# Kernel tuning notes

Hardware: AMD Instinct MI355X
Metric: run time of the kernel (lower is better)

The kernel has to match this reference:

```python
import jax, jax.numpy as jnp
import numpy as np

EPS = 1e-7
CURVS = (1.0, 0.8, 1.2)
SCALES = (1.0, 0.8, 0.6)


def expmap0(v, c):
    sc = jnp.sqrt(c)
    n = jnp.maximum(jnp.linalg.norm(v, axis=-1, keepdims=True), EPS)
    return jnp.tanh(sc * n) * v / (sc * n)


def projx(x, c):
    max_n = (1.0 - 1e-5) / jnp.sqrt(c)
    n = jnp.maximum(jnp.linalg.norm(x, axis=-1, keepdims=True), EPS)
    return jnp.where(n > max_n, x * (max_n / n), x)


def logmap0(x, c):
    sc = jnp.sqrt(c)
    n = jnp.maximum(jnp.linalg.norm(x, axis=-1, keepdims=True), EPS)
    a = jnp.clip(sc * n, 0.0, 1.0 - 1e-7)
    return jnp.arctanh(a) * x / (sc * n)


def hamilton(q1, q2):
    # q1, q2: [..., 4] (w,x,y,z), broadcasting allowed
    w1, x1, y1, z1 = q1[..., 0], q1[..., 1], q1[..., 2], q1[..., 3]
    w2, x2, y2, z2 = q2[..., 0], q2[..., 1], q2[..., 2], q2[..., 3]
    w = w1 * w2 - x1 * x2 - y1 * y2 - z1 * z2
    x = w1 * x2 + x1 * w2 + y1 * z2 - z1 * y2
    y = w1 * y2 - x1 * z2 + y1 * w2 + z1 * x2
    z = w1 * z2 + x1 * y2 - y1 * x2 + z1 * w2
    return jnp.stack([w, x, y, z], axis=-1)


def mlp(v, Wa, ba, Wb, bb):
    # Linear -> GELU(exact, matching torch default) -> Linear; dropout is eval-mode identity
    return jax.nn.gelu(v @ Wa.T + ba, approximate=False) @ Wb.T + bb


def setup_inputs() -> dict:
    key = jax.random.key(0)
    ks = jax.random.split(key, 24)
    f32 = jnp.float32
    B = 65536
    d = {}
    d['x'] = jax.random.normal(ks[0], (B, 784), dtype=f32)
    # input embedding 784 -> 128, then to level-0 tangent space 128 -> 64
    d['W_in'] = jax.random.normal(ks[1], (128, 784), f32) * (1.0 / np.sqrt(784))
    d['b_in'] = jnp.zeros((128,), f32)
    d['W_tan'] = jax.random.normal(ks[2], (64, 128), f32) * (1.0 / np.sqrt(128))
    d['b_tan'] = jnp.zeros((64,), f32)
    # boundary-manifold tangent points per level (init_scale=0.01 as in BoundaryManifold)
    d['bp0'] = jax.random.normal(ks[3], (5, 64), f32) * 0.01
    d['bp1'] = jax.random.normal(ks[4], (3, 4), f32) * 0.01
    d['bp2'] = jax.random.normal(ks[5], (4, 32), f32) * 0.01
    # rotation 0->1: SO(64) via matrix exponential of a skew-symmetric generator
    d['A_rot'] = jax.random.normal(ks[6], (64, 64), f32) * 0.02
    # rotation 1->2: SO(4) via pvq unit quaternions (std=0.1 init as in source)
    d['p_quat'] = jax.random.normal(ks[7], (4,), f32) * 0.1
    d['q_quat'] = jax.random.normal(ks[8], (4,), f32) * 0.1
    # inter-level MLP transform 0->1: 64 -> 32 -> 4
    d['W0a'] = jax.random.normal(ks[9], (32, 64), f32) * (1.0 / np.sqrt(64))
    d['b0a'] = jnp.zeros((32,), f32)
    d['W0b'] = jax.random.normal(ks[10], (4, 32), f32) * (1.0 / np.sqrt(32))
    d['b0b'] = jnp.zeros((4,), f32)
    # inter-level MLP transform 1->2: 4 -> 16 -> 32
    d['W1a'] = jax.random.normal(ks[11], (16, 4), f32) * (1.0 / np.sqrt(4))
    d['b1a'] = jnp.zeros((16,), f32)
    d['W1b'] = jax.random.normal(ks[12], (32, 16), f32) * (1.0 / np.sqrt(16))
    d['b1b'] = jnp.zeros((32,), f32)
    # output head: concat_tangent (64+4+32=100) -> 10
    d['W_out'] = jax.random.normal(ks[13], (10, 100), f32) * (1.0 / np.sqrt(100))
    d['b_out'] = jnp.zeros((10,), f32)
    return d


def reference(x, W_in, b_in, W_tan, b_tan, bp0, bp1, bp2, A_rot, p_quat, q_quat,
              W0a, b0a, W0b, b0b, W1a, b1a, W1b, b1b, W_out, b_out):
    h = x @ W_in.T + b_in                       # [B, 128]
    v = h @ W_tan.T + b_tan                     # [B, 64] level-0 tangent vector
    bps = (bp0, bp1, bp2)
    level_tangents = []
    carried = None                              # boundary tangent vectors transformed from prev level
    for i in range(3):
        c, s = CURVS[i], SCALES[i]
        # scaled exp/log round trip through the Poincare ball of this level
        x_hyp = projx(expmap0(v * s, c), c)
        v_tan = logmap0(x_hyp, c) / s           # [B, d_i]
        # boundary manifold: tangent -> ball -> proj -> tangent
        b_own = logmap0(projx(expmap0(bps[i], c), c), c)  # [P_i, d_i]
        bnds = b_own if carried is None else jnp.concatenate([b_own, carried], axis=0)
        # relative vectors vs boundary points, mean-aggregated
        rel_agg = v_tan.mean(axis=0, keepdims=False) * 0 + (v_tan[:, None, :] - bnds[None, :, :]).mean(axis=1)  # [B, d_i]
        level_tangents.append(v_tan)
        v_comb = v_tan + rel_agg
        if i == 0:
            R = jax.scipy.linalg.expm(A_rot - A_rot.T)   # SO(64)
            v_rot = v_comb @ R.T
            b_rot = bnds @ R.T
            v = mlp(v_rot, W0a, b0a, W0b, b0b)
            carried = mlp(b_rot, W0a, b0a, W0b, b0b)
        elif i == 1:
            p = p_quat / (jnp.linalg.norm(p_quat) + EPS)
            q = q_quat / (jnp.linalg.norm(q_quat) + EPS)
            v_rot = hamilton(hamilton(p, v_comb), q)     # pvq SO(4) rotation
            b_rot = hamilton(hamilton(p, bnds), q)
            v = mlp(v_rot, W1a, b1a, W1b, b1b)
            carried = mlp(b_rot, W1a, b1a, W1b, b1b)
    agg = jnp.concatenate(level_tangents, axis=-1)       # [B, 100] concat_tangent
    return agg @ W_out.T + b_out                         # [B, 10]
```

## Files before the change

kernel.cpp:

```cpp
#include <hip/hip_runtime.h>
#include <hip/hip_bf16.h>

typedef __attribute__((ext_vector_type(4))) float f32x4;
typedef __attribute__((ext_vector_type(2))) unsigned int u32x2;
typedef __attribute__((ext_vector_type(4))) unsigned int u32x4;
typedef __attribute__((ext_vector_type(8))) short bf16x8;

#define EPSF 1e-7f

__device__ __forceinline__ float radial_factor(float sumsq, float c, float s){
  float sc = sqrtf(c);
  float nv = sqrtf(sumsq);
  float nu = fmaxf(s*nv, EPSF);
  float th = tanhf(sc*nu);
  float r1 = th/sc;
  float maxn = (1.0f - 1e-5f)/sc;
  float r2 = fminf(r1, maxn);
  float n1 = fmaxf(r2, EPSF);
  float a  = fminf(sc*n1, 1.0f - 1e-7f);
  float r3 = 0.5f*logf((1.0f + a)/(1.0f - a));
  return r3*r2/(sc*n1*nu);
}

__device__ __forceinline__ float gelu_f(float x){
  return 0.5f*x*(1.0f + erff(x*0.70710678118654752f));
}

__device__ __forceinline__ unsigned f2bf1(float f){
  unsigned u = __float_as_uint(f);
  return (u + 0x7FFFu + ((u>>16)&1u)) >> 16;
}
__device__ __forceinline__ unsigned f2bf_pk(float lo, float hi){
  unsigned ul = f2bf1(lo);
  unsigned uh = __float_as_uint(hi);
  uh = (uh + 0x7FFFu + ((uh>>16)&1u)) & 0xFFFF0000u;
  return ul | uh;
}

#define WS_WC     0
#define WS_BCOMB  204800
#define WS_W0AE   205056
#define WS_BROT0  213248
#define WS_BOWN0  214528
#define WS_W0AT   215808
#define WS_MB0    224000
#define WS_MB1    224256
#define WS_W1AE   224272

__global__ __launch_bounds__(256) void prep_a(
    const float* __restrict__ W_in, const float* __restrict__ b_in,
    const float* __restrict__ W_tan, const float* __restrict__ b_tan,
    const float* __restrict__ A_rot, const float* __restrict__ W0a,
    const float* __restrict__ bp0,
    unsigned short* __restrict__ Wc, float* __restrict__ bcomb,
    float* __restrict__ W0aE, float* __restrict__ brot0, float* __restrict__ bown0)
{
  __shared__ __align__(16) float Al[64][68];
  __shared__ __align__(16) float ST[64][68];
  const int bid = blockIdx.x, t = threadIdx.x;

  if (bid < 50){
    if (bid == 0 && t < 64){
      float s = b_tan[t];
      for (int j = 0; j < 128; ++j) s += b_in[j]*W_tan[t*128+j];
      bcomb[t] = s;
    }
    const int g4 = bid*256 + t;
    const int n = g4/200, k4 = (g4 - n*200)*4;
    f32x4 s = {0.f,0.f,0.f,0.f};
    if (k4 < 784){
      for (int j = 0; j < 128; ++j){
        float wt = W_tan[n*128+j];
        f32x4 wi = *(const f32x4*)(W_in + j*784 + k4);
        s += wt*wi;
      }
    }
    u32x2 st = { f2bf_pk(s[0], s[1]), f2bf_pk(s[2], s[3]) };
    *(u32x2*)(Wc + n*800 + k4) = st;
  } else {
    for (int m = t; m < 4096; m += 256){
      int r = m >> 6, c = m & 63;
      Al[r][c] = A_rot[m];
    }
    __syncthreads();
    for (int m = t; m < 4096; m += 256){
      int r = m >> 6, c = m & 63;
      ST[r][c] = Al[c][r] - Al[r][c];
    }
    __syncthreads();
    const int wv = t >> 6, lane = t & 63;
    const int row = (bid - 50)*4 + wv;
    if (row < 37){
      float v, sgn;
      if (row < 32){ v = W0a[row*64 + lane]; sgn = 1.f; }
      else {
        const int r = row - 32;
        float b = bp0[r*64 + lane];
        float ssq = b*b;
        #pragma unroll
        for (int d = 1; d < 64; d <<= 1) ssq += __shfl_xor(ssq, d);
        float fc = radial_factor(ssq, 1.0f, 1.0f);
        v = b*fc;
        bown0[r*64 + lane] = v;
        sgn = -1.f;
      }
      float acc = v;
      for (int k = 1; k <= 12; ++k){
        const float coef = sgn/(float)k;
        float nv = 0.f;
        #pragma unroll
        for (int m = 0; m < 64; m += 4){
          f32x4 s4 = *(const f32x4*)&ST[lane][m];
          nv += __int_as_float(__builtin_amdgcn_readlane(__float_as_int(v), m+0))*s4[0];
          nv += __int_as_float(__builtin_amdgcn_readlane(__float_as_int(v), m+1))*s4[1];
          nv += __int_as_float(__builtin_amdgcn_readlane(__float_as_int(v), m+2))*s4[2];
          nv += __int_as_float(__builtin_amdgcn_readlane(__float_as_int(v), m+3))*s4[3];
        }
        nv *= coef;
        v = nv; acc += nv;
      }
      if (row < 32) W0aE[row*64 + lane] = acc;
      else          brot0[(row-32)*64 + lane] = acc;
    }
  }
}

__global__ __launch_bounds__(256) void prep_small(
    const float* __restrict__ bp1,
    const float* __restrict__ p_quat, const float* __restrict__ q_quat,
    const float* __restrict__ b0a, const float* __restrict__ W0b, const float* __restrict__ b0b,
    const float* __restrict__ W1a,
    const float* __restrict__ W0aE, const float* __restrict__ brot0, const float* __restrict__ bown0,
    float* __restrict__ W0aT, float* __restrict__ mb0, float* __restrict__ mb1,
    float* __restrict__ W1aE)
{
  __shared__ float g[5][32];
  __shared__ float c1[5][4];
  __shared__ float fac1[3];
  __shared__ float Mq[4][4];
  const int t = threadIdx.x;

  for (int i = t; i < 2048; i += 256){
    int o = i >> 6, k = i & 63;
    W0aT[k*32 + o] = W0aE[i];
  }
  if (t < 64){
    float s = 0.f;
    for (int r = 0; r < 5; ++r) s += bown0[r*64 + t];
    mb0[t] = s * 0.2f;
  }
  if (t < 160){
    int r = t >> 5, o = t & 31;
    float s = b0a[o];
    for (int k = 0; k < 64; ++k) s += brot0[r*64+k]*W0aE[o*64+k];
    g[r][o] = gelu_f(s);
  }
  if (t >= 192 && t < 195){
    int r = t - 192;
    float ssq = 0.f;
    for (int j = 0; j < 4; ++j){ float b = bp1[r*4+j]; ssq += b*b; }
    fac1[r] = radial_factor(ssq, 0.8f, 1.0f);
  }
  if (t == 224){
    float pw=p_quat[0],px=p_quat[1],py=p_quat[2],pz=p_quat[3];
    float n1 = sqrtf(pw*pw+px*px+py*py+pz*pz) + EPSF;
    pw/=n1; px/=n1; py/=n1; pz/=n1;
    float qw=q_quat[0],qx=q_quat[1],qy=q_quat[2],qz=q_quat[3];
    float n2 = sqrtf(qw*qw+qx*qx+qy*qy+qz*qz) + EPSF;
    qw/=n2; qx/=n2; qy/=n2; qz/=n2;
    float Lp[4][4] = {{pw,-px,-py,-pz},{px,pw,-pz,py},{py,pz,pw,-px},{pz,-py,px,pw}};
    float Rq[4][4] = {{qw,-qx,-qy,-qz},{qx,qw,qz,-qy},{qy,-qz,qw,qx},{qz,qy,-qx,qw}};
    #pragma unroll
    for (int i = 0; i < 4; ++i)
      #pragma unroll
      for (int k = 0; k < 4; ++k){
        float s = 0.f;
        #pragma unroll
        for (int m = 0; m < 4; ++m) s += Rq[i][m]*Lp[m][k];
        Mq[i][k] = s;
      }
  }
  __syncthreads();
  if (t < 20){
    int r = t >> 2, o = t & 3;
    float s = b0b[o];
    for (int k = 0; k < 32; ++k) s += g[r][k]*W0b[o*32+k];
    c1[r][o] = s;
  }
  __syncthreads();
  if (t < 4){
    float s = 0.f;
    for (int r = 0; r < 3; ++r) s += bp1[r*4+t]*fac1[r];
    for (int r = 0; r < 5; ++r) s += c1[r][t];
    mb1[t] = s * 0.125f;
  }
  if (t >= 64 && t < 128){
    int i = t - 64, o = i >> 2, kq = i & 3;
    float s = 0.f;
    #pragma unroll
    for (int j = 0; j < 4; ++j) s += W1a[o*4+j]*Mq[j][kq];
    W1aE[o*4+kq] = s;
  }
}

__global__ __launch_bounds__(256, 3) void main_fused(
    const float* __restrict__ x,
    const unsigned short* __restrict__ Wc,
    const float* __restrict__ bcomb,
    const float* __restrict__ W0aT,
    const float* __restrict__ mb0g, const float* __restrict__ mb1g,
    const float* __restrict__ W1aEg,
    const float* __restrict__ b0a, const float* __restrict__ W0b, const float* __restrict__ b0b,
    const float* __restrict__ b1a, const float* __restrict__ W1b, const float* __restrict__ b1b,
    const float* __restrict__ Wout, const float* __restrict__ bout,
    float* __restrict__ out)
{
  __shared__ __align__(16) char smem[49472];
  float* vlds   = (float*)smem;
  float* cWoutS = (float*)(smem + 19456);
  float* cmb0S  = (float*)(smem + 23456);
  float* cW0bS  = (float*)(smem + 23712);
  float* cW1aES = (float*)(smem + 24224);
  float* cb0aS  = (float*)(smem + 24480);
  float* cb0bS  = (float*)(smem + 24608);
  float* cmb1S  = (float*)(smem + 24624);
  float* cb1aS  = (float*)(smem + 24640);
  float* cb1bS  = (float*)(smem + 24704);
  float* cboutS = (float*)(smem + 24832);
  unsigned short* xs  = (unsigned short*)(smem + 24896);
  unsigned short* wsb = (unsigned short*)(smem + 24896 + 10240);
  float* gv     = (float*)(smem + 24896);
  float* g1     = (float*)(smem + 34112);
  float* cW0aTS = (float*)(smem + 39232);
  float* cW1bS  = (float*)(smem + 47424);

  const int tid = threadIdx.x;
  const size_t rowBase = (size_t)blockIdx.x * 64;

  if (tid < 64)  cmb0S[tid] = mb0g[tid];
  if (tid < 32)  cb0aS[tid] = b0a[tid];
  if (tid < 128) cW0bS[tid] = W0b[tid];
  if (tid < 4)   { cb0bS[tid] = b0b[tid]; cmb1S[tid] = mb1g[tid]; }
  if (tid < 64)  cW1aES[tid] = W1aEg[tid];
  if (tid < 16)  cb1aS[tid] = b1a[tid];
  if (tid < 32)  cb1bS[tid] = b1b[tid];
  if (tid < 10)  cboutS[tid] = bout[tid];
  for (int i = tid; i < 1000; i += 256) cWoutS[i] = Wout[i];

  const int lane = tid & 63;
  const int w    = tid >> 6;
  const int wr   = w >> 1, wc = w & 1;
  const int lr   = lane & 15, lkg = lane >> 4;

  const char* gpd[3]; int lod[3]; int advd[3]; int thrd[3]; int isxd[3];
  #pragma unroll
  for (int d = 0; d < 3; ++d){
    const int c = w*3 + d;
    if (c < 8){
      const int row = c*8 + (lane >> 3), seg = lane & 7;
      gpd[d]  = (const char*)(x + (rowBase + (size_t)row)*784 + seg*4);
      lod[d]  = row*40 + seg*4;
      advd[d] = 128;
      thrd[d] = 784 - seg*4;
      isxd[d] = 1;
    } else {
      const int row = (c - 8)*16 + (lane >> 2), seg = lane & 3;
      gpd[d]  = (const char*)(Wc + (size_t)row*800 + seg*8);
      lod[d]  = row*40 + seg*8;
      advd[d] = 64;
      thrd[d] = 1 << 30;
      isxd[d] = 0;
    }
  }
  const int aof0 = (wr*32 + lr)*40 + lkg*8;
  const int aof1 = aof0 + 16*40;
  const int bof0 = (wc*32 + lr)*40 + lkg*8;
  const int bof1 = bof0 + 16*40;

  #pragma unroll
  for (int d = 0; d < 3; ++d){
    u32x4 v = *(const u32x4*)gpd[d];
    gpd[d] += advd[d];
    if (isxd[d]){
      f32x4 f = __builtin_bit_cast(f32x4, v);
      u32x2 p = { f2bf_pk(f[0], f[1]), f2bf_pk(f[2], f[3]) };
      *(u32x2*)(xs + lod[d]) = p;
    } else {
      *(u32x4*)(wsb + lod[d]) = v;
    }
  }
  __syncthreads();

  f32x4 acc00 = {}, acc01 = {}, acc10 = {}, acc11 = {};
  for (int t = 0; t < 25; ++t){
    const int cur = t & 1;
    const bool have = (t < 24);
    u32x4 sv0 = {0,0,0,0}, sv1 = {0,0,0,0}, sv2 = {0,0,0,0};
    if (have){
      const int k0n = (t + 1)*32;
      if (k0n < thrd[0]) sv0 = *(const u32x4*)gpd[0];
      if (k0n < thrd[1]) sv1 = *(const u32x4*)gpd[1];
      if (k0n < thrd[2]) sv2 = *(const u32x4*)gpd[2];
      gpd[0] += advd[0]; gpd[1] += advd[1]; gpd[2] += advd[2];
    }
    const unsigned short* xc = xs  + cur*2560;
    const unsigned short* wcb = wsb + cur*2560;
    bf16x8 a0 = *(const bf16x8*)(xc  + aof0);
    bf16x8 a1 = *(const bf16x8*)(xc  + aof1);
    bf16x8 b0 = *(const bf16x8*)(wcb + bof0);
    bf16x8 b1 = *(const bf16x8*)(wcb + bof1);
    acc00 = __builtin_amdgcn_mfma_f32_16x16x32_bf16(a0, b0, acc00, 0, 0, 0);
    acc01 = __builtin_amdgcn_mfma_f32_16x16x32_bf16(a0, b1, acc01, 0, 0, 0);
    acc10 = __builtin_amdgcn_mfma_f32_16x16x32_bf16(a1, b0, acc10, 0, 0, 0);
    acc11 = __builtin_amdgcn_mfma_f32_16x16x32_bf16(a1, b1, acc11, 0, 0, 0);
    if (have){
      unsigned short* xn = xs  + (cur ^ 1)*2560;
      unsigned short* wn = wsb + (cur ^ 1)*2560;
      if (isxd[0]){ f32x4 f = __builtin_bit_cast(f32x4, sv0);
        u32x2 p = { f2bf_pk(f[0], f[1]), f2bf_pk(f[2], f[3]) }; *(u32x2*)(xn + lod[0]) = p; }
      else { *(u32x4*)(wn + lod[0]) = sv0; }
      if (isxd[1]){ f32x4 f = __builtin_bit_cast(f32x4, sv1);
        u32x2 p = { f2bf_pk(f[0], f[1]), f2bf_pk(f[2], f[3]) }; *(u32x2*)(xn + lod[1]) = p; }
      else { *(u32x4*)(wn + lod[1]) = sv1; }
      if (isxd[2]){ f32x4 f = __builtin_bit_cast(f32x4, sv2);
        u32x2 p = { f2bf_pk(f[0], f[1]), f2bf_pk(f[2], f[3]) }; *(u32x2*)(xn + lod[2]) = p; }
      else { *(u32x4*)(wn + lod[2]) = sv2; }
    }
    __syncthreads();
  }

  {
    f32x4 accA[2][2] = { {acc00, acc01}, {acc10, acc11} };
    #pragma unroll
    for (int fi = 0; fi < 2; ++fi){
      #pragma unroll
      for (int fj = 0; fj < 2; ++fj){
        const int col = wc*32 + fj*16 + lr;
        const int r0  = wr*32 + fi*16 + lkg*4;
        const float bc = bcomb[col];
        #pragma unroll
        for (int j = 0; j < 4; ++j)
          vlds[(r0 + j)*76 + col] = accA[fi][fj][j] + bc;
      }
    }
  }
  for (int i = tid; i < 2048; i += 256) cW0aTS[i] = W0aT[i];
  for (int i = tid; i < 512;  i += 256) cW1bS[i]  = W1b[i];
  __syncthreads();

  const int row = tid >> 2, p4 = tid & 3;

  {
    f32x4 rv[4];
    float* vptr = &vlds[row*76 + p4*16];
    #pragma unroll
    for (int i = 0; i < 4; ++i) rv[i] = ((const f32x4*)vptr)[i];
    float ssq = 0.f;
    #pragma unroll
    for (int i = 0; i < 4; ++i)
      ssq += rv[i][0]*rv[i][0] + rv[i][1]*rv[i][1] + rv[i][2]*rv[i][2] + rv[i][3]*rv[i][3];
    ssq += __shfl_xor(ssq, 1); ssq += __shfl_xor(ssq, 2);
    const float fac = radial_factor(ssq, 1.0f, 1.0f);
    #pragma unroll
    for (int i = 0; i < 4; ++i){ rv[i] *= fac; ((f32x4*)vptr)[i] = rv[i]; }
  }
  __syncthreads();

  {
    const int og = p4;
    float a0o[8];
    #pragma unroll
    for (int j = 0; j < 8; ++j) a0o[j] = cb0aS[og*8 + j];
    #pragma unroll 4
    for (int k = 0; k < 64; k += 4){
      f32x4 vtv = *(const f32x4*)&vlds[row*76 + k];
      f32x4 mm  = *(const f32x4*)&cmb0S[k];
      #pragma unroll
      for (int u = 0; u < 4; ++u){
        const float vc = 2.f*vtv[u] - mm[u];
        const f32x4* wp = (const f32x4*)&cW0aTS[(k+u)*32 + og*8];
        f32x4 w0 = wp[0], w1 = wp[1];
        #pragma unroll
        for (int j = 0; j < 4; ++j){ a0o[j] += w0[j]*vc; a0o[4+j] += w1[j]*vc; }
      }
    }
    #pragma unroll
    for (int j = 0; j < 8; ++j) gv[row*36 + og*8 + j] = gelu_f(a0o[j]);
  }
  __syncthreads();

  {
    const int o1 = p4;
    float a1 = cb0bS[o1];
    #pragma unroll
    for (int k = 0; k < 32; k += 4){
      f32x4 gg = *(const f32x4*)&gv[row*36 + k];
      f32x4 ww = *(const f32x4*)&cW0bS[o1*32 + k];
      a1 += gg[0]*ww[0] + gg[1]*ww[1] + gg[2]*ww[2] + gg[3]*ww[3];
    }
    float ss1 = a1*a1;
    ss1 += __shfl_xor(ss1, 1); ss1 += __shfl_xor(ss1, 2);
    const float f1v = radial_factor(ss1, 0.8f, 0.8f);
    const float vt1 = a1*f1v;
    vlds[row*76 + 64 + o1] = vt1;
    vlds[row*76 + 68 + o1] = 2.f*vt1 - cmb1S[o1];
  }
  __syncthreads();

  {
    const f32x4 vc1 = *(const f32x4*)&vlds[row*76 + 68];
    #pragma unroll
    for (int j = 0; j < 4; ++j){
      const int o = p4*4 + j;
      float s1 = cb1aS[o] + cW1aES[o*4+0]*vc1[0] + cW1aES[o*4+1]*vc1[1]
                          + cW1aES[o*4+2]*vc1[2] + cW1aES[o*4+3]*vc1[3];
      g1[row*20 + o] = gelu_f(s1);
    }
  }
  __syncthreads();

  {
    float v2[8]; float ss2 = 0.f;
    #pragma unroll
    for (int j = 0; j < 8; ++j){
      const int o = p4*8 + j;
      float s = cb1bS[o];
      #pragma unroll
      for (int k = 0; k < 16; k += 4){
        f32x4 gg = *(const f32x4*)&g1[row*20 + k];
        f32x4 ww = *(const f32x4*)&cW1bS[o*16 + k];
        s += gg[0]*ww[0] + gg[1]*ww[1] + gg[2]*ww[2] + gg[3]*ww[3];
      }
      v2[j] = s; ss2 += s*s;
    }
    ss2 += __shfl_xor(ss2, 1); ss2 += __shfl_xor(ss2, 2);
    const float f2v = radial_factor(ss2, 1.2f, 0.6f);
    #pragma unroll
    for (int j = 0; j < 8; ++j) gv[row*36 + p4*8 + j] = v2[j]*f2v;
  }
  __syncthreads();

  for (int idx = tid; idx < 640; idx += 256){
    const int r6 = idx/10, o = idx - r6*10;
    float s = cboutS[o];
    const float* wrow = &cWoutS[o*100];
    const float* vrow = &vlds[r6*76];
    #pragma unroll 4
    for (int k = 0; k < 68; k += 4){
      f32x4 a = *(const f32x4*)(vrow + k);
      f32x4 b = *(const f32x4*)(wrow + k);
      s += a[0]*b[0] + a[1]*b[1] + a[2]*b[2] + a[3]*b[3];
    }
    const float* v2row = &gv[r6*36];
    #pragma unroll 4
    for (int k = 0; k < 32; k += 4){
      f32x4 a = *(const f32x4*)(v2row + k);
      f32x4 b = *(const f32x4*)(wrow + 68 + k);
      s += a[0]*b[0] + a[1]*b[1] + a[2]*b[2] + a[3]*b[3];
    }
    out[(rowBase + (size_t)r6)*10 + o] = s;
  }
}

extern "C" void kernel_launch(void* const* d_in, const int* in_sizes, int n_in,
                              void* d_out, int out_size, void* d_ws, size_t ws_size,
                              hipStream_t stream)
{
  (void)n_in; (void)out_size; (void)ws_size;
  const float* x      = (const float*)d_in[0];
  const float* W_in   = (const float*)d_in[1];
  const float* b_in   = (const float*)d_in[2];
  const float* W_tan  = (const float*)d_in[3];
  const float* b_tan  = (const float*)d_in[4];
  const float* bp0    = (const float*)d_in[5];
  const float* bp1    = (const float*)d_in[6];
  const float* A_rot  = (const float*)d_in[8];
  const float* p_quat = (const float*)d_in[9];
  const float* q_quat = (const float*)d_in[10];
  const float* W0a    = (const float*)d_in[11];
  const float* b0a    = (const float*)d_in[12];
  const float* W0b    = (const float*)d_in[13];
  const float* b0b    = (const float*)d_in[14];
  const float* W1a    = (const float*)d_in[15];
  const float* b1a    = (const float*)d_in[16];
  const float* W1b    = (const float*)d_in[17];
  const float* b1b    = (const float*)d_in[18];
  const float* W_out  = (const float*)d_in[19];
  const float* b_out  = (const float*)d_in[20];

  char* ws = (char*)d_ws;
  unsigned short* Wc = (unsigned short*)(ws + WS_WC);
  float* bcomb = (float*)(ws + WS_BCOMB);
  float* W0aE  = (float*)(ws + WS_W0AE);
  float* brot0 = (float*)(ws + WS_BROT0);
  float* bown0 = (float*)(ws + WS_BOWN0);
  float* W0aT  = (float*)(ws + WS_W0AT);
  float* mb0   = (float*)(ws + WS_MB0);
  float* mb1   = (float*)(ws + WS_MB1);
  float* W1aE  = (float*)(ws + WS_W1AE);

  const int Brows = in_sizes[0] / 784;
  const int nblk  = Brows / 64;

  prep_a<<<60, 256, 0, stream>>>(W_in, b_in, W_tan, b_tan, A_rot, W0a, bp0,
                                 Wc, bcomb, W0aE, brot0, bown0);
  prep_small<<<1, 256, 0, stream>>>(bp1, p_quat, q_quat, b0a, W0b, b0b, W1a,
                                    W0aE, brot0, bown0, W0aT, mb0, mb1, W1aE);
  main_fused<<<nblk, 256, 0, stream>>>(x, Wc, bcomb, W0aT, mb0, mb1, W1aE,
                                       b0a, W0b, b0b, b1a, W1b, b1b,
                                       W_out, b_out, (float*)d_out);
}
```

Baseline: 89.88 us.

## Stream GEMM tiles via direct global-to-LDS loads with swizzled layouts

New measurement: 85.64 us. 1.05x faster.

```diff
diff --git a/kernel.cpp b/kernel.cpp
--- a/kernel.cpp
+++ b/kernel.cpp
@@ -37,6 +37,12 @@
   return ul | uh;
 }
 
+__device__ __forceinline__ void gload_lds16(const void* g, void* l){
+  __builtin_amdgcn_global_load_lds((const __attribute__((address_space(1))) unsigned int*)g,
+                                   (__attribute__((address_space(3))) unsigned int*)l,
+                                   16, 0, 0);
+}
+
 #define WS_WC     0
 #define WS_BCOMB  204800
 #define WS_W0AE   205056
@@ -46,6 +52,7 @@
 #define WS_MB0    224000
 #define WS_MB1    224256
 #define WS_W1AE   224272
+#define WS_ZERO   224528
 
 __global__ __launch_bounds__(256) void prep_a(
     const float* __restrict__ W_in, const float* __restrict__ b_in,
@@ -76,7 +83,11 @@
       }
     }
     u32x2 st = { f2bf_pk(s[0], s[1]), f2bf_pk(s[2], s[3]) };
-    *(u32x2*)(Wc + n*800 + k4) = st;
+    const int tsl = k4 >> 5;
+    const int q   = (k4 >> 3) & 3;
+    const int qp  = q ^ ((n >> 1) & 3);
+    const int idx = tsl*2048 + n*32 + qp*8 + (k4 & 7);
+    *(u32x2*)(Wc + idx) = st;
   } else {
     for (int m = t; m < 4096; m += 256){
       int r = m >> 6, c = m & 63;
@@ -132,7 +143,7 @@
     const float* __restrict__ W1a,
     const float* __restrict__ W0aE, const float* __restrict__ brot0, const float* __restrict__ bown0,
     float* __restrict__ W0aT, float* __restrict__ mb0, float* __restrict__ mb1,
-    float* __restrict__ W1aE)
+    float* __restrict__ W1aE, float* __restrict__ zerog)
 {
   __shared__ float g[5][32];
   __shared__ float c1[5][4];
@@ -144,6 +155,7 @@
     int o = i >> 6, k = i & 63;
     W0aT[k*32 + o] = W0aE[i];
   }
+  if (t >= 240) zerog[t - 240] = 0.f;
   if (t < 64){
     float s = 0.f;
     for (int r = 0; r < 5; ++r) s += bown0[r*64 + t];
@@ -205,7 +217,7 @@
 
 __global__ __launch_bounds__(256, 3) void main_fused(
     const float* __restrict__ x,
-    const unsigned short* __restrict__ Wc,
+    const unsigned short* __restrict__ Wcs,
     const float* __restrict__ bcomb,
     const float* __restrict__ W0aT,
     const float* __restrict__ mb0g, const float* __restrict__ mb1g,
@@ -213,30 +225,33 @@
     const float* __restrict__ b0a, const float* __restrict__ W0b, const float* __restrict__ b0b,
     const float* __restrict__ b1a, const float* __restrict__ W1b, const float* __restrict__ b1b,
     const float* __restrict__ Wout, const float* __restrict__ bout,
+    const float* __restrict__ zerog,
     float* __restrict__ out)
 {
-  __shared__ __align__(16) char smem[49472];
+  __shared__ __align__(16) char smem[49728];
   float* vlds   = (float*)smem;
   float* cWoutS = (float*)(smem + 19456);
-  float* cmb0S  = (float*)(smem + 23456);
-  float* cW0bS  = (float*)(smem + 23712);
-  float* cW1aES = (float*)(smem + 24224);
-  float* cb0aS  = (float*)(smem + 24480);
-  float* cb0bS  = (float*)(smem + 24608);
-  float* cmb1S  = (float*)(smem + 24624);
-  float* cb1aS  = (float*)(smem + 24640);
-  float* cb1bS  = (float*)(smem + 24704);
-  float* cboutS = (float*)(smem + 24832);
-  unsigned short* xs  = (unsigned short*)(smem + 24896);
-  unsigned short* wsb = (unsigned short*)(smem + 24896 + 10240);
-  float* gv     = (float*)(smem + 24896);
-  float* g1     = (float*)(smem + 34112);
-  float* cW0aTS = (float*)(smem + 39232);
-  float* cW1bS  = (float*)(smem + 47424);
+  float* cbcombS= (float*)(smem + 23456);
+  float* cmb0S  = (float*)(smem + 23712);
+  float* cW0bS  = (float*)(smem + 23968);
+  float* cW1aES = (float*)(smem + 24480);
+  float* cb0aS  = (float*)(smem + 24736);
+  float* cb0bS  = (float*)(smem + 24864);
+  float* cmb1S  = (float*)(smem + 24880);
+  float* cb1aS  = (float*)(smem + 24896);
+  float* cb1bS  = (float*)(smem + 24960);
+  float* cboutS = (float*)(smem + 25088);
+  char*  xsB    = smem + 25152;
+  char*  wcsB   = smem + 41536;
+  float* gv     = (float*)(smem + 25152);
+  float* g1     = (float*)(smem + 34368);
+  float* cW0aTS = (float*)(smem + 39488);
+  float* cW1bS  = (float*)(smem + 47680);
 
   const int tid = threadIdx.x;
   const size_t rowBase = (size_t)blockIdx.x * 64;
 
+  if (tid < 64)  cbcombS[tid] = bcomb[tid];
   if (tid < 64)  cmb0S[tid] = mb0g[tid];
   if (tid < 32)  cb0aS[tid] = b0a[tid];
   if (tid < 128) cW0bS[tid] = W0b[tid];
@@ -252,82 +267,61 @@
   const int wr   = w >> 1, wc = w & 1;
   const int lr   = lane & 15, lkg = lane >> 4;
 
-  const char* gpd[3]; int lod[3]; int advd[3]; int thrd[3]; int isxd[3];
-  #pragma unroll
-  for (int d = 0; d < 3; ++d){
-    const int c = w*3 + d;
-    if (c < 8){
-      const int row = c*8 + (lane >> 3), seg = lane & 7;
-      gpd[d]  = (const char*)(x + (rowBase + (size_t)row)*784 + seg*4);
-      lod[d]  = row*40 + seg*4;
-      advd[d] = 128;
-      thrd[d] = 784 - seg*4;
-      isxd[d] = 1;
-    } else {
-      const int row = (c - 8)*16 + (lane >> 2), seg = lane & 3;
-      gpd[d]  = (const char*)(Wc + (size_t)row*800 + seg*8);
-      lod[d]  = row*40 + seg*8;
-      advd[d] = 64;
-      thrd[d] = 1 << 30;
-      isxd[d] = 0;
-    }
-  }
-  const int aof0 = (wr*32 + lr)*40 + lkg*8;
-  const int aof1 = aof0 + 16*40;
-  const int bof0 = (wc*32 + lr)*40 + lkg*8;
-  const int bof1 = bof0 + 16*40;
-
-  #pragma unroll
-  for (int d = 0; d < 3; ++d){
-    u32x4 v = *(const u32x4*)gpd[d];
-    gpd[d] += advd[d];
-    if (isxd[d]){
-      f32x4 f = __builtin_bit_cast(f32x4, v);
-      u32x2 p = { f2bf_pk(f[0], f[1]), f2bf_pk(f[2], f[3]) };
-      *(u32x2*)(xs + lod[d]) = p;
-    } else {
-      *(u32x4*)(wsb + lod[d]) = v;
-    }
-  }
+  const int row8 = lane >> 3;
+  const int qs   = lane & 7;
+  const int qoff = qs ^ row8;
+  const float* xsrcA = x + (rowBase + (size_t)(8*w     + row8))*784 + qoff*4;
+  const float* xsrcB = x + (rowBase + (size_t)(8*(w+4) + row8))*784 + qoff*4;
+  const unsigned short* wsrc = Wcs + (16*w + (lane>>2))*32 + (lane&3)*8;
+
+  const int rA0 = wr*32 + lr;
+  const int sA0 = (2*lkg)     ^ (lr & 7);
+  const int sA1 = (2*lkg + 1) ^ (lr & 7);
+  const int offA00 = rA0*128 + sA0*16;
+  const int offA01 = rA0*128 + sA1*16;
+  const int rB0 = wc*32 + lr;
+  const int sB  = lkg ^ ((rB0 >> 1) & 3);
+  const int offB0 = rB0*64 + sB*16;
+
+#define STAGE(slab, buf) do{                                                   \
+    const int ks_ = (slab)*32;                                                 \
+    char* xd_ = xsB  + (buf)*8192;                                             \
+    char* wd_ = wcsB + (buf)*4096;                                             \
+    const float* sa_ = (ks_ + qoff*4 < 784) ? (xsrcA + ks_) : zerog;           \
+    const float* sb_ = (ks_ + qoff*4 < 784) ? (xsrcB + ks_) : zerog;           \
+    gload_lds16(sa_, xd_ + w*1024);                                            \
+    gload_lds16(sb_, xd_ + (w+4)*1024);                                        \
+    gload_lds16(wsrc + (slab)*2048, wd_ + w*1024);                             \
+  }while(0)
+
+  STAGE(0, 0);
   __syncthreads();
 
   f32x4 acc00 = {}, acc01 = {}, acc10 = {}, acc11 = {};
   for (int t = 0; t < 25; ++t){
     const int cur = t & 1;
-    const bool have = (t < 24);
-    u32x4 sv0 = {0,0,0,0}, sv1 = {0,0,0,0}, sv2 = {0,0,0,0};
-    if (have){
-      const int k0n = (t + 1)*32;
-      if (k0n < thrd[0]) sv0 = *(const u32x4*)gpd[0];
-      if (k0n < thrd[1]) sv1 = *(const u32x4*)gpd[1];
-      if (k0n < thrd[2]) sv2 = *(const u32x4*)gpd[2];
-      gpd[0] += advd[0]; gpd[1] += advd[1]; gpd[2] += advd[2];
-    }
-    const unsigned short* xc = xs  + cur*2560;
-    const unsigned short* wcb = wsb + cur*2560;
-    bf16x8 a0 = *(const bf16x8*)(xc  + aof0);
-    bf16x8 a1 = *(const bf16x8*)(xc  + aof1);
-    bf16x8 b0 = *(const bf16x8*)(wcb + bof0);
-    bf16x8 b1 = *(const bf16x8*)(wcb + bof1);
-    acc00 = __builtin_amdgcn_mfma_f32_16x16x32_bf16(a0, b0, acc00, 0, 0, 0);
-    acc01 = __builtin_amdgcn_mfma_f32_16x16x32_bf16(a0, b1, acc01, 0, 0, 0);
-    acc10 = __builtin_amdgcn_mfma_f32_16x16x32_bf16(a1, b0, acc10, 0, 0, 0);
-    acc11 = __builtin_amdgcn_mfma_f32_16x16x32_bf16(a1, b1, acc11, 0, 0, 0);
-    if (have){
-      unsigned short* xn = xs  + (cur ^ 1)*2560;
-      unsigned short* wn = wsb + (cur ^ 1)*2560;
-      if (isxd[0]){ f32x4 f = __builtin_bit_cast(f32x4, sv0);
-        u32x2 p = { f2bf_pk(f[0], f[1]), f2bf_pk(f[2], f[3]) }; *(u32x2*)(xn + lod[0]) = p; }
-      else { *(u32x4*)(wn + lod[0]) = sv0; }
-      if (isxd[1]){ f32x4 f = __builtin_bit_cast(f32x4, sv1);
-        u32x2 p = { f2bf_pk(f[0], f[1]), f2bf_pk(f[2], f[3]) }; *(u32x2*)(xn + lod[1]) = p; }
-      else { *(u32x4*)(wn + lod[1]) = sv1; }
-      if (isxd[2]){ f32x4 f = __builtin_bit_cast(f32x4, sv2);
-        u32x2 p = { f2bf_pk(f[0], f[1]), f2bf_pk(f[2], f[3]) }; *(u32x2*)(xn + lod[2]) = p; }
-      else { *(u32x4*)(wn + lod[2]) = sv2; }
-    }
+    if (t < 24) STAGE(t+1, cur^1);
+    const char* xb = xsB  + cur*8192;
+    const char* wb = wcsB + cur*4096;
+    f32x4 a00 = *(const f32x4*)(xb + offA00);
+    f32x4 a01 = *(const f32x4*)(xb + offA01);
+    f32x4 a10 = *(const f32x4*)(xb + offA00 + 2048);
+    f32x4 a11 = *(const f32x4*)(xb + offA01 + 2048);
+    bf16x8 b0 = *(const bf16x8*)(wb + offB0);
+    bf16x8 b1 = *(const bf16x8*)(wb + offB0 + 1024);
+    u32x4 pk0 = { f2bf_pk(a00[0],a00[1]), f2bf_pk(a00[2],a00[3]),
+                  f2bf_pk(a01[0],a01[1]), f2bf_pk(a01[2],a01[3]) };
+    u32x4 pk1 = { f2bf_pk(a10[0],a10[1]), f2bf_pk(a10[2],a10[3]),
+                  f2bf_pk(a11[0],a11[1]), f2bf_pk(a11[2],a11[3]) };
+    bf16x8 af0 = __builtin_bit_cast(bf16x8, pk0);
+    bf16x8 af1 = __builtin_bit_cast(bf16x8, pk1);
+    acc00 = __builtin_amdgcn_mfma_f32_16x16x32_bf16(af0, b0, acc00, 0, 0, 0);
+    acc01 = __builtin_amdgcn_mfma_f32_16x16x32_bf16(af0, b1, acc01, 0, 0, 0);
+    acc10 = __builtin_amdgcn_mfma_f32_16x16x32_bf16(af1, b0, acc10, 0, 0, 0);
+    acc11 = __builtin_amdgcn_mfma_f32_16x16x32_bf16(af1, b1, acc11, 0, 0, 0);
     __syncthreads();
   }
+#undef STAGE
 
   {
     f32x4 accA[2][2] = { {acc00, acc01}, {acc10, acc11} };
@@ -337,7 +331,7 @@
       for (int fj = 0; fj < 2; ++fj){
         const int col = wc*32 + fj*16 + lr;
         const int r0  = wr*32 + fi*16 + lkg*4;
-        const float bc = bcomb[col];
+        const float bc = cbcombS[col];
         #pragma unroll
         for (int j = 0; j < 4; ++j)
           vlds[(r0 + j)*76 + col] = accA[fi][fj][j] + bc;
@@ -489,7 +483,7 @@
   const float* b_out  = (const float*)d_in[20];
 
   char* ws = (char*)d_ws;
-  unsigned short* Wc = (unsigned short*)(ws + WS_WC);
+  unsigned short* Wcs = (unsigned short*)(ws + WS_WC);
   float* bcomb = (float*)(ws + WS_BCOMB);
   float* W0aE  = (float*)(ws + WS_W0AE);
   float* brot0 = (float*)(ws + WS_BROT0);
@@ -498,15 +492,16 @@
   float* mb0   = (float*)(ws + WS_MB0);
   float* mb1   = (float*)(ws + WS_MB1);
   float* W1aE  = (float*)(ws + WS_W1AE);
+  float* zerog = (float*)(ws + WS_ZERO);
 
   const int Brows = in_sizes[0] / 784;
   const int nblk  = Brows / 64;
 
   prep_a<<<60, 256, 0, stream>>>(W_in, b_in, W_tan, b_tan, A_rot, W0a, bp0,
-                                 Wc, bcomb, W0aE, brot0, bown0);
+                                 Wcs, bcomb, W0aE, brot0, bown0);
   prep_small<<<1, 256, 0, stream>>>(bp1, p_quat, q_quat, b0a, W0b, b0b, W1a,
-                                    W0aE, brot0, bown0, W0aT, mb0, mb1, W1aE);
-  main_fused<<<nblk, 256, 0, stream>>>(x, Wc, bcomb, W0aT, mb0, mb1, W1aE,
+                                    W0aE, brot0, bown0, W0aT, mb0, mb1, W1aE, zerog);
+  main_fused<<<nblk, 256, 0, stream>>>(x, Wcs, bcomb, W0aT, mb0, mb1, W1aE,
                                        b0a, W0b, b0b, b1a, W1b, b1b,
-                                       W_out, b_out, (float*)d_out);
-}
+                                       W_out, b_out, zerog, (float*)d_out);
+}
```
